# Kernel optimization log

Measured on AMD Instinct MI355X. Metric: run time of the kernel, lower is better.

The kernel has to match this reference:

```python
import jax, jax.numpy as jnp
import numpy as np

N_NODES = 50000
N_EDGES = 800000
IN_C, HID_C, OUT_C = 512, 256, 2


def gcn_conv(x, W, b, src, dst, norm, num_nodes):
    # x: [N, Fin]; W: [Fin, Fout]; src/dst/norm: [E+N] (self-loops included)
    h = x @ W                                   # [N, Fout]
    msgs = h[src] * norm[:, None]               # gather + scale, [E+N, Fout]
    out = jax.ops.segment_sum(msgs, dst, num_segments=num_nodes)  # scatter-add
    return out + b


def _gcn_norm(src, dst, num_nodes):
    # PyG gcn_norm with add_self_loops=True, unit edge weights
    loop = jnp.arange(num_nodes, dtype=src.dtype)
    src2 = jnp.concatenate([src, loop])
    dst2 = jnp.concatenate([dst, loop])
    w = jnp.ones(src2.shape[0], dtype=jnp.float32)
    deg = jax.ops.segment_sum(w, dst2, num_segments=num_nodes)
    dinv = jnp.where(deg > 0, jax.lax.rsqrt(deg), 0.0)
    norm = dinv[src2] * dinv[dst2]
    return src2, dst2, norm


def setup_inputs() -> dict:
    key = jax.random.key(0)
    ks = jax.random.split(key, 4)
    x = jax.random.normal(ks[0], (N_NODES, IN_C), dtype=jnp.float32)
    edge_index = jax.random.randint(ks[1], (2, N_EDGES), 0, N_NODES, dtype=jnp.int64)
    W1 = jax.random.normal(ks[2], (IN_C, HID_C), dtype=jnp.float32) / np.sqrt(IN_C)
    b1 = jnp.zeros((HID_C,), dtype=jnp.float32)
    W2 = jax.random.normal(ks[3], (HID_C, OUT_C), dtype=jnp.float32) / np.sqrt(HID_C)
    b2 = jnp.zeros((OUT_C,), dtype=jnp.float32)
    return {"x": x, "edge_index": edge_index, "W1": W1, "b1": b1, "W2": W2, "b2": b2}


def reference(x, edge_index, W1, b1, W2, b2):
    n = x.shape[0]
    src, dst, norm = _gcn_norm(edge_index[0], edge_index[1], n)
    h = gcn_conv(x, W1, b1, src, dst, norm, n)
    h = jax.nn.relu(h)
    # dropout is identity in eval mode (training=False)
    out = gcn_conv(h, W2, b2, src, dst, norm, n)
    return out
```

## Files before the change

### kernel.cpp

```cpp
#include <hip/hip_runtime.h>
#include <hip/hip_bf16.h>
#include <stdint.h>

#define N_NODES 50000
#define N_EDGES 800000
#define IN_C 512
#define HID_C 256
#define CAP 96

typedef __attribute__((ext_vector_type(8))) short bf16x8;
typedef __attribute__((ext_vector_type(4))) float f32x4;
typedef __attribute__((address_space(3))) uint32_t lds_u32_t;
typedef __attribute__((address_space(1))) const uint32_t g_u32_t;

__device__ __forceinline__ void g2l16(const void* g, void* l) {
    __builtin_amdgcn_global_load_lds((g_u32_t*)g, (lds_u32_t*)l, 16, 0, 0);
}

__device__ __forceinline__ unsigned short f2bf(float f) {
    uint32_t u = __float_as_uint(f);
    uint32_t r = (u + 0x7fff + ((u >> 16) & 1)) >> 16;
    return (unsigned short)r;
}


#define ZERO_BLOCKS ((N_NODES + 255) / 256)
#define PREP_BLOCKS (ZERO_BLOCKS + 256)

__global__ __launch_bounds__(256) void prep_kernel(int* __restrict__ cursor,
                                                   const float* __restrict__ W1,
                                                   unsigned short* __restrict__ Wt) {
    const int t = threadIdx.x;
    if (blockIdx.x < ZERO_BLOCKS) {
        const int i = blockIdx.x * 256 + t;
        if (i < N_NODES) cursor[i] = 0;
    } else {
        const int c = blockIdx.x - ZERO_BLOCKS;
        for (int k = t; k < IN_C; k += 256)
            Wt[c * IN_C + k] = f2bf(W1[k * HID_C + c]);
    }
}


#define GEMM_BLOCKS ((N_NODES + 127) / 128)
#define FILL_BLOCKS ((N_EDGES + 1023) / 1024)
#define GF_BLOCKS (GEMM_BLOCKS + FILL_BLOCKS)
#define NKT 16

__global__ __launch_bounds__(512) void gf_kernel(
    const float* __restrict__ A,
    const unsigned short* __restrict__ Bt,
    unsigned short* __restrict__ hB,
    int M,
    const int* __restrict__ src,
    const int* __restrict__ dst,
    int* cursor,
    int* __restrict__ bucket)
{
    __shared__ float          Asf[2][128 * 32];
    __shared__ unsigned short Bs[2][256 * 32];
    const int t = threadIdx.x;

    if (blockIdx.x >= GEMM_BLOCKS) {
        const int i0 = ((blockIdx.x - GEMM_BLOCKS) * 512 + t) * 2;
        if (i0 >= N_EDGES) return;
        int s0, d0, s1 = -1, d1 = -1;
        if (i0 + 2 <= N_EDGES) {
            const int2 s2 = *(const int2*)&src[i0];
            const int2 d2 = *(const int2*)&dst[i0];
            s0 = s2.x; s1 = s2.y; d0 = d2.x; d1 = d2.y;
        } else {
            s0 = src[i0]; d0 = dst[i0];
        }
        const int p0 = atomicAdd(&cursor[d0], 1);
        if (p0 < CAP) bucket[d0 * CAP + p0] = s0;
        if (s1 >= 0) {
            const int p1 = atomicAdd(&cursor[d1], 1);
            if (p1 < CAP) bucket[d1 * CAP + p1] = s1;
        }
        return;
    }

    const int m0 = blockIdx.x * 128;
    const int w = t >> 6, l = t & 63;
    const int wr = (w >> 2) * 64;
    const int wc = (w & 3) * 64;
    const int l15 = l & 15, l4 = l >> 4;

    f32x4 acc[4][4] = {};

    auto stage = [&](int buf, int kt) {
        #pragma unroll
        for (int q = 0; q < 2; ++q) {
            const int idx = q * 512 + t;
            const int row = idx >> 3;
            const int ck  = (idx & 7) ^ (row & 7);
            int gr = m0 + row; if (gr >= M) gr = M - 1;
            g2l16(&A[(size_t)gr * IN_C + kt * 32 + ck * 4], &Asf[buf][idx * 4]);
        }
        #pragma unroll
        for (int q = 0; q < 2; ++q) {
            const int idx = q * 512 + t;
            const int row = idx >> 2;
            const int ck  = (idx & 3) ^ (row & 3) ^ ((row >> 2) & 3);
            g2l16(&Bt[(size_t)row * IN_C + kt * 32 + ck * 8], &Bs[buf][idx * 8]);
        }
    };
    auto compute = [&](int buf) {
        bf16x8 a[4], b[4];
        #pragma unroll
        for (int mi = 0; mi < 4; ++mi) {
            const int r  = wr + mi * 16 + l15;
            const int s0 = l4 * 2;
            const float4 lo = *(const float4*)&Asf[buf][r * 32 + ((s0    ) ^ (r & 7)) * 4];
            const float4 hi = *(const float4*)&Asf[buf][r * 32 + ((s0 + 1) ^ (r & 7)) * 4];
            union { bf16x8 v; __hip_bfloat162 h2[4]; } cv;
            cv.h2[0] = __float22bfloat162_rn(make_float2(lo.x, lo.y));
            cv.h2[1] = __float22bfloat162_rn(make_float2(lo.z, lo.w));
            cv.h2[2] = __float22bfloat162_rn(make_float2(hi.x, hi.y));
            cv.h2[3] = __float22bfloat162_rn(make_float2(hi.z, hi.w));
            a[mi] = cv.v;
        }
        #pragma unroll
        for (int nj = 0; nj < 4; ++nj) {
            const int r  = wc + nj * 16 + l15;
            const int ck = l4 ^ (r & 3) ^ ((r >> 2) & 3);
            b[nj] = *(const bf16x8*)&Bs[buf][r * 32 + ck * 8];
        }
        #pragma unroll
        for (int mi = 0; mi < 4; ++mi)
            #pragma unroll
            for (int nj = 0; nj < 4; ++nj)
                acc[mi][nj] = __builtin_amdgcn_mfma_f32_16x16x32_bf16(
                    a[mi], b[nj], acc[mi][nj], 0, 0, 0);
    };

    stage(0, 0);
    asm volatile("s_waitcnt vmcnt(0)" ::: "memory");
    __builtin_amdgcn_s_barrier();
    int cur = 0;
    for (int kt = 0; kt < NKT; ++kt) {
        if (kt < NKT - 1) {
            stage(cur ^ 1, kt + 1);
            asm volatile("s_waitcnt vmcnt(4)" ::: "memory");
        } else {
            asm volatile("s_waitcnt vmcnt(0)" ::: "memory");
        }
        __builtin_amdgcn_s_barrier();
        compute(cur);
        __builtin_amdgcn_s_barrier();
        cur ^= 1;
    }

    #pragma unroll
    for (int mi = 0; mi < 4; ++mi)
        #pragma unroll
        for (int nj = 0; nj < 4; ++nj)
            #pragma unroll
            for (int rr = 0; rr < 4; ++rr) {
                const int m = m0 + wr + mi * 16 + l4 * 4 + rr;
                const int n = wc + nj * 16 + l15;
                if (m < M) hB[(size_t)m * HID_C + n] = f2bf(acc[mi][nj][rr]);
            }
}


__global__ void dinv_kernel(const int* __restrict__ cursor,
                            float* __restrict__ dinv, int n) {
    const int i = blockIdx.x * 256 + threadIdx.x;
    if (i < n) dinv[i] = rsqrtf((float)(cursor[i] + 1));
}


__device__ __forceinline__ void fma8(float* acc, uint4 r, float w) {
    acc[0] += __uint_as_float((r.x & 0xffffu) << 16) * w;
    acc[1] += __uint_as_float(r.x & 0xffff0000u) * w;
    acc[2] += __uint_as_float((r.y & 0xffffu) << 16) * w;
    acc[3] += __uint_as_float(r.y & 0xffff0000u) * w;
    acc[4] += __uint_as_float((r.z & 0xffffu) << 16) * w;
    acc[5] += __uint_as_float(r.z & 0xffff0000u) * w;
    acc[6] += __uint_as_float((r.w & 0xffffu) << 16) * w;
    acc[7] += __uint_as_float(r.w & 0xffff0000u) * w;
}

__global__ __launch_bounds__(256) void agg1_kernel(const unsigned short* __restrict__ h,
                                                   const int* __restrict__ cursor,
                                                   const int* __restrict__ bucket,
                                                   const float* __restrict__ dinv,
                                                   const float* __restrict__ b1,
                                                   const float* __restrict__ W2,
                                                   float* __restrict__ h2) {
    const int node = blockIdx.x * 8 + (threadIdx.x >> 5);
    const int g = threadIdx.x & 31;
    const int f0 = g << 3;
    int cnt = cursor[node]; if (cnt > CAP) cnt = CAP;
    const float dv_d = dinv[node];

    float acc[8] = {};
    {
        const uint4 rs = *(const uint4*)&h[(size_t)node * HID_C + f0];
        fma8(acc, rs, dv_d);
    }

    const int* bkt = &bucket[node * CAP];
    for (int base = 0; base < cnt; base += 32) {
        const int rem = cnt - base;
        const int c32 = rem < 32 ? rem : 32;
        int idx = 0; float dv_s = 0.f;
        if (g < c32) {
            idx  = bkt[base + g];
            dv_s = dinv[idx];
        }
        int i = 0;
        for (; i + 4 <= c32; i += 4) {
            const int   i0 = __shfl(idx, i,     32); const float w0 = __shfl(dv_s, i,     32);
            const int   i1 = __shfl(idx, i + 1, 32); const float w1 = __shfl(dv_s, i + 1, 32);
            const int   i2 = __shfl(idx, i + 2, 32); const float w2 = __shfl(dv_s, i + 2, 32);
            const int   i3 = __shfl(idx, i + 3, 32); const float w3 = __shfl(dv_s, i + 3, 32);
            const uint4 r0 = *(const uint4*)&h[(size_t)i0 * HID_C + f0];
            const uint4 r1 = *(const uint4*)&h[(size_t)i1 * HID_C + f0];
            const uint4 r2 = *(const uint4*)&h[(size_t)i2 * HID_C + f0];
            const uint4 r3 = *(const uint4*)&h[(size_t)i3 * HID_C + f0];
            fma8(acc, r0, w0); fma8(acc, r1, w1); fma8(acc, r2, w2); fma8(acc, r3, w3);
        }
        for (; i < c32; ++i) {
            const int   ii = __shfl(idx, i, 32);
            const float w  = __shfl(dv_s, i, 32);
            const uint4 r  = *(const uint4*)&h[(size_t)ii * HID_C + f0];
            fma8(acc, r, w);
        }
    }

    const float4 ba = *(const float4*)&b1[f0];
    const float4 bb = *(const float4*)&b1[f0 + 4];
    float v[8];
    v[0] = fmaxf(acc[0] * dv_d + ba.x, 0.f); v[1] = fmaxf(acc[1] * dv_d + ba.y, 0.f);
    v[2] = fmaxf(acc[2] * dv_d + ba.z, 0.f); v[3] = fmaxf(acc[3] * dv_d + ba.w, 0.f);
    v[4] = fmaxf(acc[4] * dv_d + bb.x, 0.f); v[5] = fmaxf(acc[5] * dv_d + bb.y, 0.f);
    v[6] = fmaxf(acc[6] * dv_d + bb.z, 0.f); v[7] = fmaxf(acc[7] * dv_d + bb.w, 0.f);

    float c0 = 0.f, c1 = 0.f;
    #pragma unroll
    for (int q = 0; q < 4; ++q) {
        const float4 wv = *(const float4*)&W2[f0 * 2 + q * 4];
        c0 += v[2*q] * wv.x + v[2*q+1] * wv.z;
        c1 += v[2*q] * wv.y + v[2*q+1] * wv.w;
    }
    #pragma unroll
    for (int o = 16; o > 0; o >>= 1) {
        c0 += __shfl_down(c0, o, 32);
        c1 += __shfl_down(c1, o, 32);
    }
    if (g == 0) *(float2*)&h2[node * 2] = make_float2(c0, c1);
}


__global__ void agg2_kernel(const float* __restrict__ h2,
                            const int* __restrict__ cursor,
                            const int* __restrict__ bucket,
                            const float* __restrict__ dinv,
                            const float* __restrict__ b2,
                            float* __restrict__ out, int n_nodes) {
    const int n = blockIdx.x * blockDim.x + threadIdx.x;
    if (n >= n_nodes) return;
    int cnt = cursor[n]; if (cnt > CAP) cnt = CAP;
    const float dv_d = dinv[n];
    const float2 ps = *(const float2*)&h2[n * 2];
    float a0 = dv_d * ps.x, a1 = dv_d * ps.y;
    const int* bkt = &bucket[n * CAP];
    int i = 0;
    for (; i + 4 <= cnt; i += 4) {
        const int4 s4 = *(const int4*)&bkt[i];
        const float w0 = dinv[s4.x], w1 = dinv[s4.y];
        const float w2 = dinv[s4.z], w3 = dinv[s4.w];
        const float2 p0 = *(const float2*)&h2[s4.x * 2];
        const float2 p1 = *(const float2*)&h2[s4.y * 2];
        const float2 p2 = *(const float2*)&h2[s4.z * 2];
        const float2 p3 = *(const float2*)&h2[s4.w * 2];
        a0 += p0.x * w0 + p1.x * w1 + p2.x * w2 + p3.x * w3;
        a1 += p0.y * w0 + p1.y * w1 + p2.y * w2 + p3.y * w3;
    }
    for (; i < cnt; ++i) {
        const int s = bkt[i];
        const float w = dinv[s];
        const float2 p = *(const float2*)&h2[s * 2];
        a0 += p.x * w;
        a1 += p.y * w;
    }
    out[n * 2 + 0] = b2[0] + dv_d * a0;
    out[n * 2 + 1] = b2[1] + dv_d * a1;
}


static inline size_t align_up(size_t x) { return (x + 255) & ~(size_t)255; }

extern "C" void kernel_launch(void* const* d_in, const int* in_sizes, int n_in,
                              void* d_out, int out_size, void* d_ws, size_t ws_size,
                              hipStream_t stream) {
    const float* x   = (const float*)d_in[0];
    const int*   ei  = (const int*)d_in[1];
    const float* W1  = (const float*)d_in[2];
    const float* b1  = (const float*)d_in[3];
    const float* W2  = (const float*)d_in[4];
    const float* b2  = (const float*)d_in[5];
    float* out = (float*)d_out;

    const int* e_src = ei;
    const int* e_dst = ei + N_EDGES;

    char* ws = (char*)d_ws;
    int*   cursor   = (int*)ws;             ws += align_up((size_t)N_NODES * 4);
    float* dinv     = (float*)ws;           ws += align_up((size_t)N_NODES * 4);
    int*   bucket   = (int*)ws;             ws += align_up((size_t)N_NODES * CAP * 4);
    unsigned short* Wt = (unsigned short*)ws; ws += align_up((size_t)HID_C * IN_C * 2);
    unsigned short* h  = (unsigned short*)ws; ws += align_up((size_t)N_NODES * HID_C * 2);
    float* h2       = (float*)ws;           ws += align_up((size_t)N_NODES * 2 * 4);

    const int nb_n = (N_NODES + 255) / 256;

    prep_kernel<<<PREP_BLOCKS, 256, 0, stream>>>(cursor, W1, Wt);
    gf_kernel<<<GF_BLOCKS, 512, 0, stream>>>(x, Wt, h, N_NODES,
                                             e_src, e_dst, cursor, bucket);
    dinv_kernel<<<nb_n, 256, 0, stream>>>(cursor, dinv, N_NODES);
    agg1_kernel<<<N_NODES / 8, 256, 0, stream>>>(h, cursor, bucket, dinv, b1, W2, h2);
    agg2_kernel<<<nb_n, 256, 0, stream>>>(h2, cursor, bucket, dinv, b2, out, N_NODES);
}
```

Baseline: 128.3 us.

## Single-buffer B tile in GEMM, reorder fill blocks first with one edge per thread

Shrinks the B tile in shared memory from double to single buffering, cutting LDS use so more GEMM blocks can be resident. A is still prefetched one step ahead, but B for the next step is now loaded only after compute and waited on with a full vmcnt(0) before the next iteration, which exposes B load latency. The edge bucket-fill blocks are moved ahead of the GEMM blocks in the grid and now handle one edge per thread instead of two, so the atomic-heavy fill work is scheduled first.

After: 162.0 us. 26.3% more time.

```diff
diff --git a/kernel.cpp b/kernel.cpp
--- a/kernel.cpp
+++ b/kernel.cpp
@@ -42,9 +42,9 @@
 }
 
 
+#define FILL_BLOCKS ((N_EDGES + 511) / 512)
 #define GEMM_BLOCKS ((N_NODES + 127) / 128)
-#define FILL_BLOCKS ((N_EDGES + 1023) / 1024)
-#define GF_BLOCKS (GEMM_BLOCKS + FILL_BLOCKS)
+#define GF_BLOCKS (FILL_BLOCKS + GEMM_BLOCKS)
 #define NKT 16
 
 __global__ __launch_bounds__(512) void gf_kernel(
@@ -58,30 +58,20 @@
     int* __restrict__ bucket)
 {
     __shared__ float          Asf[2][128 * 32];
-    __shared__ unsigned short Bs[2][256 * 32];
+    __shared__ unsigned short Bs[256 * 32];
     const int t = threadIdx.x;
 
-    if (blockIdx.x >= GEMM_BLOCKS) {
-        const int i0 = ((blockIdx.x - GEMM_BLOCKS) * 512 + t) * 2;
-        if (i0 >= N_EDGES) return;
-        int s0, d0, s1 = -1, d1 = -1;
-        if (i0 + 2 <= N_EDGES) {
-            const int2 s2 = *(const int2*)&src[i0];
-            const int2 d2 = *(const int2*)&dst[i0];
-            s0 = s2.x; s1 = s2.y; d0 = d2.x; d1 = d2.y;
-        } else {
-            s0 = src[i0]; d0 = dst[i0];
-        }
-        const int p0 = atomicAdd(&cursor[d0], 1);
-        if (p0 < CAP) bucket[d0 * CAP + p0] = s0;
-        if (s1 >= 0) {
-            const int p1 = atomicAdd(&cursor[d1], 1);
-            if (p1 < CAP) bucket[d1 * CAP + p1] = s1;
-        }
+    if (blockIdx.x < FILL_BLOCKS) {
+        const int i = blockIdx.x * 512 + t;
+        if (i >= N_EDGES) return;
+        const int s = src[i];
+        const int d = dst[i];
+        const int p = atomicAdd(&cursor[d], 1);
+        if (p < CAP) bucket[d * CAP + p] = s;
         return;
     }
 
-    const int m0 = blockIdx.x * 128;
+    const int m0 = (blockIdx.x - FILL_BLOCKS) * 128;
     const int w = t >> 6, l = t & 63;
     const int wr = (w >> 2) * 64;
     const int wc = (w & 3) * 64;
@@ -89,7 +79,7 @@
 
     f32x4 acc[4][4] = {};
 
-    auto stage = [&](int buf, int kt) {
+    auto stageA = [&](int buf, int kt) {
         #pragma unroll
         for (int q = 0; q < 2; ++q) {
             const int idx = q * 512 + t;
@@ -98,12 +88,14 @@
             int gr = m0 + row; if (gr >= M) gr = M - 1;
             g2l16(&A[(size_t)gr * IN_C + kt * 32 + ck * 4], &Asf[buf][idx * 4]);
         }
+    };
+    auto stageB = [&](int kt) {
         #pragma unroll
         for (int q = 0; q < 2; ++q) {
             const int idx = q * 512 + t;
             const int row = idx >> 2;
             const int ck  = (idx & 3) ^ (row & 3) ^ ((row >> 2) & 3);
-            g2l16(&Bt[(size_t)row * IN_C + kt * 32 + ck * 8], &Bs[buf][idx * 8]);
+            g2l16(&Bt[(size_t)row * IN_C + kt * 32 + ck * 8], &Bs[idx * 8]);
         }
     };
     auto compute = [&](int buf) {
@@ -125,7 +117,7 @@
         for (int nj = 0; nj < 4; ++nj) {
             const int r  = wc + nj * 16 + l15;
             const int ck = l4 ^ (r & 3) ^ ((r >> 2) & 3);
-            b[nj] = *(const bf16x8*)&Bs[buf][r * 32 + ck * 8];
+            b[nj] = *(const bf16x8*)&Bs[r * 32 + ck * 8];
         }
         #pragma unroll
         for (int mi = 0; mi < 4; ++mi)
@@ -135,19 +127,16 @@
                     a[mi], b[nj], acc[mi][nj], 0, 0, 0);
     };
 
-    stage(0, 0);
+    stageA(0, 0); stageB(0);
     asm volatile("s_waitcnt vmcnt(0)" ::: "memory");
     __builtin_amdgcn_s_barrier();
     int cur = 0;
     for (int kt = 0; kt < NKT; ++kt) {
-        if (kt < NKT - 1) {
-            stage(cur ^ 1, kt + 1);
-            asm volatile("s_waitcnt vmcnt(4)" ::: "memory");
-        } else {
-            asm volatile("s_waitcnt vmcnt(0)" ::: "memory");
-        }
+        if (kt < NKT - 1) stageA(cur ^ 1, kt + 1);
+        compute(cur);
         __builtin_amdgcn_s_barrier();
-        compute(cur);
+        if (kt < NKT - 1) stageB(kt + 1);
+        asm volatile("s_waitcnt vmcnt(0)" ::: "memory");
         __builtin_amdgcn_s_barrier();
         cur ^= 1;
     }
```
